# Kernel optimization log

Hardware: AMD Instinct MI355X
Metric: run time of the kernel (lower is better)

The kernel has to match this reference:

```python
import jax, jax.numpy as jnp
import numpy as np


def setup_inputs() -> dict:
    key = jax.random.key(0)
    ks = jax.random.split(key, 4)
    B, H, W, C = 4, 64, 64, 64
    d = C // 8
    s = 0.05
    return {
        "x": jax.random.normal(ks[0], (B, H, W, C), dtype=jnp.float32),
        "Wq": jax.random.normal(ks[1], (C, d), dtype=jnp.float32) * s,
        "bq": jnp.zeros((d,), dtype=jnp.float32),
        "Wk": jax.random.normal(ks[2], (C, d), dtype=jnp.float32) * s,
        "bk": jnp.zeros((d,), dtype=jnp.float32),
        "Wv": jax.random.normal(ks[3], (C, C), dtype=jnp.float32) * s,
        "bv": jnp.zeros((C,), dtype=jnp.float32),
        "gamma": jnp.zeros((1,), dtype=jnp.float32),
    }


def reference(x, Wq, bq, Wk, bk, Wv, bv, gamma):
    B, H, W, C = x.shape
    N = H * W
    xt = x.reshape(B, N, C)  # tokens = flattened spatial positions
    # 1x1 convs == per-token matmuls
    q = xt @ Wq + bq          # [B, N, C//8]
    k = xt @ Wk + bk          # [B, N, C//8]
    v = xt @ Wv + bv          # [B, N, C]
    # unscaled QK^T softmax (SAGAN uses no 1/sqrt(d) scaling)
    attn = jax.nn.softmax(jnp.einsum('bnd,bmd->bnm', q, k), axis=-1)  # [B, N, N]
    out = jnp.einsum('bnm,bmc->bnc', attn, v).reshape(B, H, W, C)
    return gamma * out + x
```

## Files before the change

kernel.cpp:

```cpp
#include <hip/hip_runtime.h>
#include <hip/hip_bf16.h>


typedef __attribute__((ext_vector_type(4))) float f32x4;

#define LOG2E 1.44269504088896340736f

#if __has_builtin(__builtin_amdgcn_exp2f)
#define EXP2(x) __builtin_amdgcn_exp2f(x)
#else
#define EXP2(x) __builtin_exp2f(x)
#endif

__device__ __forceinline__ unsigned short f2bf(float f) {
    __hip_bfloat16 h = __float2bfloat16(f);
    union { __hip_bfloat16 h; unsigned short u; } cv;
    cv.h = h;
    return cv.u;
}

__device__ __forceinline__ float bf2f(unsigned short u) {
    union { unsigned int i; float f; } cv;
    cv.i = ((unsigned int)u) << 16;
    return cv.f;
}

__global__ __launch_bounds__(256) void sagan_proj_kernel(
    const float* __restrict__ x,
    const float* __restrict__ Wq, const float* __restrict__ bq,
    const float* __restrict__ Wk, const float* __restrict__ bk,
    const float* __restrict__ Wv, const float* __restrict__ bv,
    unsigned char* __restrict__ Q8, unsigned char* __restrict__ K8,
    unsigned char* __restrict__ V8, unsigned char* __restrict__ zp)
{
    __shared__ float xs[32][68];
    const int tid = threadIdx.x;
    const int blk = blockIdx.x;
    const int tglob0 = blk << 5;
    const int b  = tglob0 >> 12;
    const int nb = tglob0 & 4095;

    if (blk == 0 && tid < 16) zp[tid] = 0;

    {
        const int t = tid >> 3, q8i = tid & 7;
        const float* src = x + (size_t)(tglob0 + t) * 64 + q8i * 8;
        *(f32x4*)&xs[t][q8i * 8]     = *(const f32x4*)(src);
        *(f32x4*)&xs[t][q8i * 8 + 4] = *(const f32x4*)(src + 4);
    }
    __syncthreads();

    {
        const int c  = tid & 63;
        const int tg = tid >> 6;
        float wcol[64];
        #pragma unroll
        for (int cc = 0; cc < 64; ++cc) wcol[cc] = Wv[cc * 64 + c];
        const float bvc = bv[c];
        float vacc[8];
        #pragma unroll
        for (int j = 0; j < 8; ++j) {
            const int tok = tg * 8 + j;
            float acc = bvc;
            #pragma unroll
            for (int c4 = 0; c4 < 16; ++c4) {
                f32x4 xv = *(const f32x4*)&xs[tok][c4 * 4];
                acc += xv[0] * wcol[c4 * 4 + 0] + xv[1] * wcol[c4 * 4 + 1]
                     + xv[2] * wcol[c4 * 4 + 2] + xv[3] * wcol[c4 * 4 + 3];
            }
            vacc[j] = acc;
        }
        int i0 = __builtin_amdgcn_cvt_pk_fp8_f32(vacc[0], vacc[1], 0, false);
        i0     = __builtin_amdgcn_cvt_pk_fp8_f32(vacc[2], vacc[3], i0, true);
        int i1 = __builtin_amdgcn_cvt_pk_fp8_f32(vacc[4], vacc[5], 0, false);
        i1     = __builtin_amdgcn_cvt_pk_fp8_f32(vacc[6], vacc[7], i1, true);
        unsigned char* dst = V8 + ((size_t)((b * 128 + (nb >> 5)) * 64 + c)) * 32
                                + tg * 8;
        *(uint2*)dst = make_uint2((unsigned int)i0, (unsigned int)i1);
    }

    if (tid < 128) {
        const int tok = tid >> 2;
        const int dp  = (tid & 3) * 2;
        float q0 = bq[dp], q1 = bq[dp + 1];
        float k0 = bk[dp], k1 = bk[dp + 1];
        #pragma unroll
        for (int cc = 0; cc < 64; ++cc) {
            const float xv = xs[tok][cc];
            const float2 wq = *(const float2*)&Wq[cc * 8 + dp];
            const float2 wk = *(const float2*)&Wk[cc * 8 + dp];
            q0 += xv * wq.x; q1 += xv * wq.y;
            k0 += xv * wk.x; k1 += xv * wk.y;
        }
        const size_t toff = (size_t)(tglob0 + tok) * 8 + dp;
        const int qi = __builtin_amdgcn_cvt_pk_fp8_f32(q0 * LOG2E, q1 * LOG2E, 0, false);
        const int ki = __builtin_amdgcn_cvt_pk_fp8_f32(k0, k1, 0, false);
        *(unsigned short*)(Q8 + toff) = (unsigned short)(qi & 0xFFFF);
        *(unsigned short*)(K8 + toff) = (unsigned short)(ki & 0xFFFF);
    }
}


#define QTILE(KA0, KA1, QF, LL, A0, A1, A2, A3, VF0, VF1, VF2, VF3) do {      \
    const f32x4 zc = {0.f, 0.f, 0.f, 0.f};                                    \
    f32x4 s0 = __builtin_amdgcn_mfma_f32_16x16x32_fp8_fp8(KA0, QF, zc, 0,0,0);\
    f32x4 s1 = __builtin_amdgcn_mfma_f32_16x16x32_fp8_fp8(KA1, QF, zc, 0,0,0);\
    float p[8];                                                               \
    _Pragma("unroll")                                                         \
    for (int r = 0; r < 4; ++r) {                                             \
        p[r]     = EXP2(s0[r]);                                               \
        p[4 + r] = EXP2(s1[r]);                                               \
    }                                                                         \
    LL += ((p[0] + p[1]) + (p[2] + p[3])) + ((p[4] + p[5]) + (p[6] + p[7]));  \
    union { int i[2]; long l; } pa;                                           \
    pa.i[0] = __builtin_amdgcn_cvt_pk_fp8_f32(p[0], p[1], 0, false);          \
    pa.i[0] = __builtin_amdgcn_cvt_pk_fp8_f32(p[2], p[3], pa.i[0], true);     \
    pa.i[1] = __builtin_amdgcn_cvt_pk_fp8_f32(p[4], p[5], 0, false);          \
    pa.i[1] = __builtin_amdgcn_cvt_pk_fp8_f32(p[6], p[7], pa.i[1], true);     \
    A0 = __builtin_amdgcn_mfma_f32_16x16x32_fp8_fp8(pa.l, VF0, A0, 0, 0, 0);  \
    A1 = __builtin_amdgcn_mfma_f32_16x16x32_fp8_fp8(pa.l, VF1, A1, 0, 0, 0);  \
    A2 = __builtin_amdgcn_mfma_f32_16x16x32_fp8_fp8(pa.l, VF2, A2, 0, 0, 0);  \
    A3 = __builtin_amdgcn_mfma_f32_16x16x32_fp8_fp8(pa.l, VF3, A3, 0, 0, 0);  \
} while (0)

__global__ __launch_bounds__(1024, 4) void sagan_flash_kernel(
    const unsigned char* __restrict__ Q8, const unsigned char* __restrict__ K8,
    const unsigned char* __restrict__ V8, const unsigned char* __restrict__ zp,
    const float* __restrict__ x, const float* __restrict__ gamma_p,
    float* __restrict__ out)
{
    __shared__ unsigned short sacc[16][64][72];
    __shared__ float sl[16][64];

    const int tid  = threadIdx.x;
    const int lane = tid & 63;
    const int w    = tid >> 6;
    const int g    = lane >> 4;
    const int ql   = lane & 15;
    const int blk  = blockIdx.x;
    const int b    = blk >> 6;
    const int qbase = (blk & 63) << 6;

    const unsigned char* Kbase = K8 + (size_t)b * (4096 * 8);
    const unsigned char* Qbase = Q8 + (size_t)b * (4096 * 8);

    long qf0, qf1, qf2, qf3;
    {
        const unsigned char* qp = Qbase + (size_t)(qbase + ql) * 8;
        qf0 = (g == 0) ? *(const long*)(qp)       : 0L;
        qf1 = (g == 0) ? *(const long*)(qp + 128) : 0L;
        qf2 = (g == 0) ? *(const long*)(qp + 256) : 0L;
        qf3 = (g == 0) ? *(const long*)(qp + 384) : 0L;
    }

    const int kt0 = w << 8;

    const unsigned char* kp0;
    int kstep;
    if (g == 0) {
        const int kperm = ((ql >> 2) << 3) | (ql & 3);
        kp0 = Kbase + (size_t)(kt0 + kperm) * 8;
        kstep = 256;
    } else {
        kp0 = zp; kstep = 0;
    }

    const unsigned char* vp = V8 + (size_t)(b * 128 + w * 8) * 2048
                                 + ql * 32 + g * 8;

    f32x4 acc00 = {0.f,0.f,0.f,0.f}, acc01 = acc00, acc02 = acc00, acc03 = acc00;
    f32x4 acc10 = acc00, acc11 = acc00, acc12 = acc00, acc13 = acc00;
    f32x4 acc20 = acc00, acc21 = acc00, acc22 = acc00, acc23 = acc00;
    f32x4 acc30 = acc00, acc31 = acc00, acc32 = acc00, acc33 = acc00;
    float l0 = 0.f, l1 = 0.f, l2 = 0.f, l3 = 0.f;

    #pragma unroll 1
    for (int it = 0; it < 8; ++it) {
        const long ka0 = *(const long*)kp0;
        const long ka1 = *(const long*)(kp0 + 32);
        kp0 += kstep;
        const long vf0 = *(const long*)(vp);
        const long vf1 = *(const long*)(vp + 512);
        const long vf2 = *(const long*)(vp + 1024);
        const long vf3 = *(const long*)(vp + 1536);
        vp += 2048;

        __builtin_amdgcn_s_setprio(1);
        QTILE(ka0, ka1, qf0, l0, acc00, acc01, acc02, acc03, vf0, vf1, vf2, vf3);
        QTILE(ka0, ka1, qf1, l1, acc10, acc11, acc12, acc13, vf0, vf1, vf2, vf3);
        QTILE(ka0, ka1, qf2, l2, acc20, acc21, acc22, acc23, vf0, vf1, vf2, vf3);
        QTILE(ka0, ka1, qf3, l3, acc30, acc31, acc32, acc33, vf0, vf1, vf2, vf3);
        __builtin_amdgcn_s_setprio(0);
    }

    l0 += __shfl_xor(l0, 16); l0 += __shfl_xor(l0, 32);
    l1 += __shfl_xor(l1, 16); l1 += __shfl_xor(l1, 32);
    l2 += __shfl_xor(l2, 16); l2 += __shfl_xor(l2, 32);
    l3 += __shfl_xor(l3, 16); l3 += __shfl_xor(l3, 32);

    #pragma unroll
    for (int r = 0; r < 4; ++r) {
        const int row = (g << 2) | r;
        unsigned short* d0 = &sacc[w][row][0];
        d0[ql] = f2bf(acc00[r]); d0[16 + ql] = f2bf(acc01[r]);
        d0[32 + ql] = f2bf(acc02[r]); d0[48 + ql] = f2bf(acc03[r]);
        unsigned short* d1 = &sacc[w][16 + row][0];
        d1[ql] = f2bf(acc10[r]); d1[16 + ql] = f2bf(acc11[r]);
        d1[32 + ql] = f2bf(acc12[r]); d1[48 + ql] = f2bf(acc13[r]);
        unsigned short* d2 = &sacc[w][32 + row][0];
        d2[ql] = f2bf(acc20[r]); d2[16 + ql] = f2bf(acc21[r]);
        d2[32 + ql] = f2bf(acc22[r]); d2[48 + ql] = f2bf(acc23[r]);
        unsigned short* d3 = &sacc[w][48 + row][0];
        d3[ql] = f2bf(acc30[r]); d3[16 + ql] = f2bf(acc31[r]);
        d3[32 + ql] = f2bf(acc32[r]); d3[48 + ql] = f2bf(acc33[r]);
    }
    if (g == 0) {
        sl[w][ql] = l0; sl[w][16 + ql] = l1;
        sl[w][32 + ql] = l2; sl[w][48 + ql] = l3;
    }
    __syncthreads();

    {
        const int row = tid >> 4;
        const int c0  = tid & 15;
        float L = 0.f, O0 = 0.f, O1 = 0.f, O2 = 0.f, O3 = 0.f;
        #pragma unroll
        for (int ww = 0; ww < 16; ++ww) {
            L += sl[ww][row];
            const unsigned short* s = &sacc[ww][row][0];
            O0 += bf2f(s[c0]);      O1 += bf2f(s[c0 + 16]);
            O2 += bf2f(s[c0 + 32]); O3 += bf2f(s[c0 + 48]);
        }
        const float Li = 1.0f / L;
        const float gm = gamma_p[0];
        const size_t rowoff = ((size_t)(b * 4096 + qbase + row)) * 64;
        out[rowoff + c0]      = gm * (O0 * Li) + x[rowoff + c0];
        out[rowoff + c0 + 16] = gm * (O1 * Li) + x[rowoff + c0 + 16];
        out[rowoff + c0 + 32] = gm * (O2 * Li) + x[rowoff + c0 + 32];
        out[rowoff + c0 + 48] = gm * (O3 * Li) + x[rowoff + c0 + 48];
    }
}

extern "C" void kernel_launch(void* const* d_in, const int* in_sizes, int n_in,
                              void* d_out, int out_size, void* d_ws, size_t ws_size,
                              hipStream_t stream) {
    const float* x  = (const float*)d_in[0];
    const float* Wq = (const float*)d_in[1];
    const float* bq = (const float*)d_in[2];
    const float* Wk = (const float*)d_in[3];
    const float* bk = (const float*)d_in[4];
    const float* Wv = (const float*)d_in[5];
    const float* bv = (const float*)d_in[6];
    const float* gm = (const float*)d_in[7];
    float* out = (float*)d_out;

    unsigned char* Q8 = (unsigned char*)d_ws;
    unsigned char* K8 = Q8 + 131072;
    unsigned char* V8 = K8 + 131072;
    unsigned char* zp = V8 + 1048576;

    hipLaunchKernelGGL(sagan_proj_kernel, dim3(512), dim3(256), 0, stream,
                       x, Wq, bq, Wk, bk, Wv, bv, Q8, K8, V8, zp);
    hipLaunchKernelGGL(sagan_flash_kernel, dim3(256), dim3(1024), 0, stream,
                       Q8, K8, V8, zp, x, gm, out);
}
```

Baseline: 31.56 us.

## Halve query tile per block, use 8 waves over longer key ranges, vectorize epilogue

Each block now handles 32 query rows with 8 waves instead of 64 rows with 16 waves, and each wave covers 512 keys over 16 iterations instead of 256 over 8. The grid doubles to 512 blocks to spread work over more CUs and cut the cross-wave reduction and shared-memory footprint. The epilogue now reads packed bf16 pairs and does 128-bit loads and stores of x and out. The trade-off is that each K/V chunk is reused across only 2 query tiles instead of 4, so K/V loads rise relative to compute.

```diff
diff --git a/kernel.cpp b/kernel.cpp
--- a/kernel.cpp
+++ b/kernel.cpp
@@ -123,14 +123,14 @@
     A3 = __builtin_amdgcn_mfma_f32_16x16x32_fp8_fp8(pa.l, VF3, A3, 0, 0, 0);  \
 } while (0)
 
-__global__ __launch_bounds__(1024, 4) void sagan_flash_kernel(
+__global__ __launch_bounds__(512, 4) void sagan_flash_kernel(
     const unsigned char* __restrict__ Q8, const unsigned char* __restrict__ K8,
     const unsigned char* __restrict__ V8, const unsigned char* __restrict__ zp,
     const float* __restrict__ x, const float* __restrict__ gamma_p,
     float* __restrict__ out)
 {
-    __shared__ unsigned short sacc[16][64][72];
-    __shared__ float sl[16][64];
+    __shared__ unsigned short sacc[8][32][72];
+    __shared__ float sl[8][32];
 
     const int tid  = threadIdx.x;
     const int lane = tid & 63;
@@ -138,22 +138,20 @@
     const int g    = lane >> 4;
     const int ql   = lane & 15;
     const int blk  = blockIdx.x;
-    const int b    = blk >> 6;
-    const int qbase = (blk & 63) << 6;
+    const int b    = blk >> 7;
+    const int qbase = (blk & 127) << 5;
 
     const unsigned char* Kbase = K8 + (size_t)b * (4096 * 8);
     const unsigned char* Qbase = Q8 + (size_t)b * (4096 * 8);
 
-    long qf0, qf1, qf2, qf3;
+    long qf0, qf1;
     {
         const unsigned char* qp = Qbase + (size_t)(qbase + ql) * 8;
         qf0 = (g == 0) ? *(const long*)(qp)       : 0L;
         qf1 = (g == 0) ? *(const long*)(qp + 128) : 0L;
-        qf2 = (g == 0) ? *(const long*)(qp + 256) : 0L;
-        qf3 = (g == 0) ? *(const long*)(qp + 384) : 0L;
-    }
-
-    const int kt0 = w << 8;
+    }
+
+    const int kt0 = w << 9;
 
     const unsigned char* kp0;
     int kstep;
@@ -165,17 +163,15 @@
         kp0 = zp; kstep = 0;
     }
 
-    const unsigned char* vp = V8 + (size_t)(b * 128 + w * 8) * 2048
+    const unsigned char* vp = V8 + (size_t)(b * 128 + w * 16) * 2048
                                  + ql * 32 + g * 8;
 
     f32x4 acc00 = {0.f,0.f,0.f,0.f}, acc01 = acc00, acc02 = acc00, acc03 = acc00;
     f32x4 acc10 = acc00, acc11 = acc00, acc12 = acc00, acc13 = acc00;
-    f32x4 acc20 = acc00, acc21 = acc00, acc22 = acc00, acc23 = acc00;
-    f32x4 acc30 = acc00, acc31 = acc00, acc32 = acc00, acc33 = acc00;
-    float l0 = 0.f, l1 = 0.f, l2 = 0.f, l3 = 0.f;
+    float l0 = 0.f, l1 = 0.f;
 
     #pragma unroll 1
-    for (int it = 0; it < 8; ++it) {
+    for (int it = 0; it < 16; ++it) {
         const long ka0 = *(const long*)kp0;
         const long ka1 = *(const long*)(kp0 + 32);
         kp0 += kstep;
@@ -188,15 +184,11 @@
         __builtin_amdgcn_s_setprio(1);
         QTILE(ka0, ka1, qf0, l0, acc00, acc01, acc02, acc03, vf0, vf1, vf2, vf3);
         QTILE(ka0, ka1, qf1, l1, acc10, acc11, acc12, acc13, vf0, vf1, vf2, vf3);
-        QTILE(ka0, ka1, qf2, l2, acc20, acc21, acc22, acc23, vf0, vf1, vf2, vf3);
-        QTILE(ka0, ka1, qf3, l3, acc30, acc31, acc32, acc33, vf0, vf1, vf2, vf3);
         __builtin_amdgcn_s_setprio(0);
     }
 
     l0 += __shfl_xor(l0, 16); l0 += __shfl_xor(l0, 32);
     l1 += __shfl_xor(l1, 16); l1 += __shfl_xor(l1, 32);
-    l2 += __shfl_xor(l2, 16); l2 += __shfl_xor(l2, 32);
-    l3 += __shfl_xor(l3, 16); l3 += __shfl_xor(l3, 32);
 
     #pragma unroll
     for (int r = 0; r < 4; ++r) {
@@ -207,37 +199,36 @@
         unsigned short* d1 = &sacc[w][16 + row][0];
         d1[ql] = f2bf(acc10[r]); d1[16 + ql] = f2bf(acc11[r]);
         d1[32 + ql] = f2bf(acc12[r]); d1[48 + ql] = f2bf(acc13[r]);
-        unsigned short* d2 = &sacc[w][32 + row][0];
-        d2[ql] = f2bf(acc20[r]); d2[16 + ql] = f2bf(acc21[r]);
-        d2[32 + ql] = f2bf(acc22[r]); d2[48 + ql] = f2bf(acc23[r]);
-        unsigned short* d3 = &sacc[w][48 + row][0];
-        d3[ql] = f2bf(acc30[r]); d3[16 + ql] = f2bf(acc31[r]);
-        d3[32 + ql] = f2bf(acc32[r]); d3[48 + ql] = f2bf(acc33[r]);
     }
     if (g == 0) {
         sl[w][ql] = l0; sl[w][16 + ql] = l1;
-        sl[w][32 + ql] = l2; sl[w][48 + ql] = l3;
     }
     __syncthreads();
 
     {
         const int row = tid >> 4;
-        const int c0  = tid & 15;
-        float L = 0.f, O0 = 0.f, O1 = 0.f, O2 = 0.f, O3 = 0.f;
-        #pragma unroll
-        for (int ww = 0; ww < 16; ++ww) {
+        const int c4  = tid & 15;
+        float L = 0.f;
+        float O[4] = {0.f, 0.f, 0.f, 0.f};
+        #pragma unroll
+        for (int ww = 0; ww < 8; ++ww) {
             L += sl[ww][row];
-            const unsigned short* s = &sacc[ww][row][0];
-            O0 += bf2f(s[c0]);      O1 += bf2f(s[c0 + 16]);
-            O2 += bf2f(s[c0 + 32]); O3 += bf2f(s[c0 + 48]);
+            const uint2 v = *(const uint2*)&sacc[ww][row][c4 * 4];
+            O[0] += bf2f((unsigned short)(v.x & 0xFFFF));
+            O[1] += bf2f((unsigned short)(v.x >> 16));
+            O[2] += bf2f((unsigned short)(v.y & 0xFFFF));
+            O[3] += bf2f((unsigned short)(v.y >> 16));
         }
         const float Li = 1.0f / L;
         const float gm = gamma_p[0];
-        const size_t rowoff = ((size_t)(b * 4096 + qbase + row)) * 64;
-        out[rowoff + c0]      = gm * (O0 * Li) + x[rowoff + c0];
-        out[rowoff + c0 + 16] = gm * (O1 * Li) + x[rowoff + c0 + 16];
-        out[rowoff + c0 + 32] = gm * (O2 * Li) + x[rowoff + c0 + 32];
-        out[rowoff + c0 + 48] = gm * (O3 * Li) + x[rowoff + c0 + 48];
+        const size_t off = ((size_t)(b * 4096 + qbase + row)) * 64 + c4 * 4;
+        const f32x4 xv = *(const f32x4*)(x + off);
+        f32x4 o;
+        o[0] = gm * (O[0] * Li) + xv[0];
+        o[1] = gm * (O[1] * Li) + xv[1];
+        o[2] = gm * (O[2] * Li) + xv[2];
+        o[3] = gm * (O[3] * Li) + xv[3];
+        *(f32x4*)(out + off) = o;
     }
 }
 
@@ -261,6 +252,6 @@
 
     hipLaunchKernelGGL(sagan_proj_kernel, dim3(512), dim3(256), 0, stream,
                        x, Wq, bq, Wk, bk, Wv, bv, Q8, K8, V8, zp);
-    hipLaunchKernelGGL(sagan_flash_kernel, dim3(256), dim3(1024), 0, stream,
+    hipLaunchKernelGGL(sagan_flash_kernel, dim3(512), dim3(512), 0, stream,
                        Q8, K8, V8, zp, x, gm, out);
 }
```

New measurement: 30.10 us. 4.6% less time.
